# Optimization experiments

Measured on AMD Instinct MI355X. Metric: run time of the kernel, lower is better.

Reference implementation:

```python
import jax, jax.numpy as jnp
import numpy as np

N_NODES = 100000
N_EDGES = 1600000
IN_CH = 128
NF = 128
OUT_CH = 3
N_LAYERS = 7
SLOPE = 0.02


def _glorot(key, shape):
    fan_in = shape[-1]
    bound = 1.0 / np.sqrt(fan_in)
    return jax.random.uniform(key, shape, jnp.float32, -bound, bound)


def setup_inputs() -> dict:
    key = jax.random.key(0)
    ks = jax.random.split(key, 10)
    x = jax.random.normal(ks[0], (N_NODES, IN_CH), jnp.float32)
    edge_index = jax.random.randint(ks[1], (2, N_EDGES), 0, N_NODES, jnp.int64 if jax.config.jax_enable_x64 else jnp.int32)
    # 7 hidden SAGEConv layers (in=128 == nf=128, so stackable)
    Wl = _glorot(ks[2], (N_LAYERS, NF, NF))   # neighbor-branch weight (lin_l)
    bl = jnp.zeros((N_LAYERS, NF), jnp.float32)
    Wr = _glorot(ks[3], (N_LAYERS, NF, NF))   # root weight (lin_r, no bias)
    # output SAGEConv: nf -> out_channels
    Wl_out = _glorot(ks[4], (OUT_CH, NF))
    bl_out = jnp.zeros((OUT_CH,), jnp.float32)
    Wr_out = _glorot(ks[5], (OUT_CH, NF))
    return {"x": x, "edge_index": edge_index, "Wl": Wl, "bl": bl, "Wr": Wr,
            "Wl_out": Wl_out, "bl_out": bl_out, "Wr_out": Wr_out}


def _leaky(v):
    return jnp.where(v >= 0, v, SLOPE * v)


def _sage_conv(h, src, dst, Wl, bl, Wr, n_nodes):
    # max-aggregate neighbor features: gather x_j = h[src], scatter-max into dst
    agg = jax.ops.segment_max(h[src], dst, num_segments=n_nodes)  # [N, C]
    agg = jnp.where(jnp.isneginf(agg), 0.0, agg)  # isolated nodes -> 0 (PyG convention)
    return agg @ Wl.T + bl + h @ Wr.T


def reference(x, edge_index, Wl, bl, Wr, Wl_out, bl_out, Wr_out):
    n = x.shape[0]
    src, dst = edge_index[0], edge_index[1]
    h = x
    # PyG BasicGNN: activation between layers, none after the last conv
    for i in range(N_LAYERS):
        h = _sage_conv(h, src, dst, Wl[i], bl[i], Wr[i], n)
        if i < N_LAYERS - 1:
            h = _leaky(h)
    # wrapper: leaky_relu, dropout (eval -> identity), final SAGEConv, tanh*0.5
    h = _leaky(h)
    h = _sage_conv(h, src, dst, Wl_out, bl_out, Wr_out, n)
    return jnp.tanh(h) * 0.5
```

## Files before the change

kernel.cpp:

```cpp
#include <hip/hip_runtime.h>
#include <hip/hip_bf16.h>
#include <math.h>

#define NN 100000
#define NE 1600000
#define NFE 128
#define SCAN_NB 98

using f32x4 = __attribute__((ext_vector_type(4))) float;
using s16x8 = __attribute__((ext_vector_type(8))) short;
using s16x4 = __attribute__((ext_vector_type(4))) short;

__device__ __forceinline__ short bf16_rne(float x) {
  unsigned u = __float_as_uint(x);
  unsigned r = u + 0x7FFFu + ((u >> 16) & 1u);
  return (short)(r >> 16);
}
__device__ __forceinline__ float bf16_f(short s) {
  return __uint_as_float(((unsigned)(unsigned short)s) << 16);
}
__device__ __forceinline__ float leaky(float v) {
  return v >= 0.0f ? v : 0.02f * v;
}
__device__ __forceinline__ float4 fmax4(float4 a, float4 b) {
  return make_float4(fmaxf(a.x, b.x), fmaxf(a.y, b.y), fmaxf(a.z, b.z), fmaxf(a.w, b.w));
}


__global__ __launch_bounds__(256) void k_zero_i32(int* __restrict__ p, int n) {
  int i = blockIdx.x * blockDim.x + threadIdx.x;
  if (i < n) p[i] = 0;
}

__global__ __launch_bounds__(256) void k_hist(const int* __restrict__ dst,
                                              int* __restrict__ counts) {
  int e = blockIdx.x * blockDim.x + threadIdx.x;
  if (e < NE) atomicAdd(&counts[dst[e]], 1);
}

__global__ __launch_bounds__(256) void k_scan_sum(const int* __restrict__ counts,
                                                  int* __restrict__ bsum) {
  const int t = threadIdx.x;
  const int base = blockIdx.x * 1024 + t * 4;
  int4 c = make_int4(0, 0, 0, 0);
  if (base + 3 < NN) c = *(const int4*)(counts + base);
  else {
    if (base + 0 < NN) c.x = counts[base + 0];
    if (base + 1 < NN) c.y = counts[base + 1];
    if (base + 2 < NN) c.z = counts[base + 2];
  }
  int s = c.x + c.y + c.z + c.w;
#pragma unroll
  for (int off = 32; off; off >>= 1) s += __shfl_down(s, off, 64);
  __shared__ int ws[4];
  if ((t & 63) == 0) ws[t >> 6] = s;
  __syncthreads();
  if (t == 0) bsum[blockIdx.x] = ws[0] + ws[1] + ws[2] + ws[3];
}

__global__ __launch_bounds__(128) void k_scan_top(const int* __restrict__ bsum,
                                                  int* __restrict__ boff) {
  __shared__ int v[128];
  const int t = threadIdx.x;
  int mine = (t < SCAN_NB) ? bsum[t] : 0;
  v[t] = mine;
  __syncthreads();
  for (int off = 1; off < 128; off <<= 1) {
    int u = (t >= off) ? v[t - off] : 0;
    __syncthreads();
    v[t] += u;
    __syncthreads();
  }
  if (t < SCAN_NB) boff[t] = v[t] - mine;
}

__global__ __launch_bounds__(256) void k_scan_blk(const int* __restrict__ counts,
                                                  const int* __restrict__ boff,
                                                  int* __restrict__ row_ptr,
                                                  int* __restrict__ cursor) {
  __shared__ int part[256];
  const int t = threadIdx.x;
  const int base = blockIdx.x * 1024 + t * 4;
  int4 c = make_int4(0, 0, 0, 0);
  if (base + 3 < NN) c = *(const int4*)(counts + base);
  else {
    if (base + 0 < NN) c.x = counts[base + 0];
    if (base + 1 < NN) c.y = counts[base + 1];
    if (base + 2 < NN) c.z = counts[base + 2];
  }
  const int s = c.x + c.y + c.z + c.w;
  part[t] = s;
  __syncthreads();
  for (int off = 1; off < 256; off <<= 1) {
    int u = (t >= off) ? part[t - off] : 0;
    __syncthreads();
    part[t] += u;
    __syncthreads();
  }
  int excl = boff[blockIdx.x] + part[t] - s;
  int4 r;
  r.x = excl;
  r.y = r.x + c.x;
  r.z = r.y + c.y;
  r.w = r.z + c.z;
  const int4 z = make_int4(0, 0, 0, 0);
  if (base + 3 < NN) {
    *(int4*)(row_ptr + base) = r;
    *(int4*)(cursor + base) = z;
  } else {
    if (base + 0 < NN) { row_ptr[base + 0] = r.x; cursor[base + 0] = 0; }
    if (base + 1 < NN) { row_ptr[base + 1] = r.y; cursor[base + 1] = 0; }
    if (base + 2 < NN) { row_ptr[base + 2] = r.z; cursor[base + 2] = 0; }
  }
  if (blockIdx.x == 0 && t == 0) row_ptr[NN] = NE;
}

__global__ __launch_bounds__(256) void k_fill(const int* __restrict__ src,
                                              const int* __restrict__ dst,
                                              const int* __restrict__ row_ptr,
                                              int* __restrict__ cursor,
                                              int* __restrict__ nbr) {
  int e = blockIdx.x * blockDim.x + threadIdx.x;
  if (e >= NE) return;
  int d = dst[e];
  int p = atomicAdd(&cursor[d], 1);
  nbr[row_ptr[d] + p] = src[e];
}


__global__ __launch_bounds__(256) void k_prep_w(const float* __restrict__ Wl,
                                                const float* __restrict__ Wr,
                                                short* __restrict__ wb) {
  int idx = blockIdx.x * 256 + threadIdx.x;
  if (idx >= 7 * 2 * 16384) return;
  int li = idx / 32768;
  int rem = idx % 32768;
  int seg = rem / 16384;
  int ok = rem % 16384;
  float v = seg ? Wr[li * 16384 + ok] : Wl[li * 16384 + ok];
  short hi = bf16_rne(v);
  short lo = bf16_rne(v - bf16_f(hi));
  short* base = wb + (size_t)li * 65536 + seg * 32768;
  base[ok] = hi;
  base[16384 + ok] = lo;
}


__global__ __launch_bounds__(256) void k_layer_fused(const float* __restrict__ hin,
                                                     const int* __restrict__ row_ptr,
                                                     const int* __restrict__ nbr,
                                                     const short* __restrict__ wbl,
                                                     const float* __restrict__ bl,
                                                     float* __restrict__ hout) {
  __shared__ __align__(16) char smem[4 * 8192];
  const int t = threadIdx.x;
  const int base = blockIdx.x * 32;

  {
    char* dhi = smem + 2 * 8192;
    char* dlo = smem + 3 * 8192;
#pragma unroll
    for (int i = 0; i < 2; ++i) {
      int c = t + 256 * i;
      int row = c >> 4;
      int kc = (c & 15) * 8;
      const float4* g = (const float4*)(hin + (size_t)(base + row) * NFE + kc);
      float4 v0 = g[0], v1 = g[1];
      float f[8] = {v0.x, v0.y, v0.z, v0.w, v1.x, v1.y, v1.z, v1.w};
      s16x8 hv, lv;
#pragma unroll
      for (int j = 0; j < 8; ++j) {
        short h = bf16_rne(f[j]);
        hv[j] = h;
        lv[j] = bf16_rne(f[j] - bf16_f(h));
      }
      int off = row * 256 + kc * 2;
      off ^= (row & 7) << 4;
      *(s16x8*)(dhi + off) = hv;
      *(s16x8*)(dlo + off) = lv;
    }
  }

  {
    char* ahi = smem;
    char* alo = smem + 8192;
    const int grp = t >> 5;
    const int lg = t & 31;
    const int c4 = lg << 2;
    const float NI = __int_as_float(0xFF800000);
#pragma unroll
    for (int ni = 0; ni < 4; ++ni) {
      const int r = grp * 4 + ni;
      const int n = base + r;
      const int start = row_ptr[n], end = row_ptr[n + 1];
      float4 acc = make_float4(NI, NI, NI, NI);
      int j = start;
      for (; j + 4 <= end; j += 4) {
        int s0 = nbr[j], s1 = nbr[j + 1], s2 = nbr[j + 2], s3 = nbr[j + 3];
        float4 v0 = *(const float4*)(hin + (size_t)s0 * NFE + c4);
        float4 v1 = *(const float4*)(hin + (size_t)s1 * NFE + c4);
        float4 v2 = *(const float4*)(hin + (size_t)s2 * NFE + c4);
        float4 v3 = *(const float4*)(hin + (size_t)s3 * NFE + c4);
        acc = fmax4(acc, fmax4(fmax4(v0, v1), fmax4(v2, v3)));
      }
      for (; j < end; ++j) {
        int s = nbr[j];
        acc = fmax4(acc, *(const float4*)(hin + (size_t)s * NFE + c4));
      }
      if (start == end) acc = make_float4(0.f, 0.f, 0.f, 0.f);
      float f[4] = {acc.x, acc.y, acc.z, acc.w};
      s16x4 hv, lv;
#pragma unroll
      for (int q = 0; q < 4; ++q) {
        short h = bf16_rne(f[q]);
        hv[q] = h;
        lv[q] = bf16_rne(f[q] - bf16_f(h));
      }
      int off = r * 256 + c4 * 2;
      off ^= (r & 7) << 4;
      *(s16x4*)(ahi + off) = hv;
      *(s16x4*)(alo + off) = lv;
    }
  }
  __syncthreads();

  const int w = t >> 6;
  const int l = t & 63;
  const int lr = l & 15;
  const int lk = (l >> 4) * 8;

  f32x4 acc[2][2] = {};

#pragma unroll
  for (int seg = 0; seg < 2; ++seg) {
    const char* ahi = smem + (seg * 2 + 0) * 8192;
    const char* alo = smem + (seg * 2 + 1) * 8192;
    const short* bhb = wbl + seg * 32768;
    const short* blb = wbl + seg * 32768 + 16384;
#pragma unroll
    for (int ks = 0; ks < 4; ++ks) {
      const int k0 = ks * 32;
      int offa0 = (lr) * 256 + (k0 + lk) * 2;      offa0 ^= ((lr) & 7) << 4;
      int offa1 = (16 + lr) * 256 + (k0 + lk) * 2; offa1 ^= ((16 + lr) & 7) << 4;
      s16x8 ah0 = *(const s16x8*)(ahi + offa0);
      s16x8 ah1 = *(const s16x8*)(ahi + offa1);
      s16x8 al0 = *(const s16x8*)(alo + offa0);
      s16x8 al1 = *(const s16x8*)(alo + offa1);
#pragma unroll
      for (int ct = 0; ct < 2; ++ct) {
        const int col = w * 32 + ct * 16 + lr;
        const s16x8 bh = *(const s16x8*)(bhb + col * 128 + k0 + lk);
        const s16x8 bl_ = *(const s16x8*)(blb + col * 128 + k0 + lk);
        acc[0][ct] = __builtin_amdgcn_mfma_f32_16x16x32_bf16(ah0, bh, acc[0][ct], 0, 0, 0);
        acc[1][ct] = __builtin_amdgcn_mfma_f32_16x16x32_bf16(ah1, bh, acc[1][ct], 0, 0, 0);
        acc[0][ct] = __builtin_amdgcn_mfma_f32_16x16x32_bf16(ah0, bl_, acc[0][ct], 0, 0, 0);
        acc[1][ct] = __builtin_amdgcn_mfma_f32_16x16x32_bf16(ah1, bl_, acc[1][ct], 0, 0, 0);
        acc[0][ct] = __builtin_amdgcn_mfma_f32_16x16x32_bf16(al0, bh, acc[0][ct], 0, 0, 0);
        acc[1][ct] = __builtin_amdgcn_mfma_f32_16x16x32_bf16(al1, bh, acc[1][ct], 0, 0, 0);
      }
    }
  }

  const float bias0 = bl[w * 32 + lr];
  const float bias1 = bl[w * 32 + 16 + lr];
#pragma unroll
  for (int rt = 0; rt < 2; ++rt) {
#pragma unroll
    for (int r = 0; r < 4; ++r) {
      int node = base + 16 * rt + (l >> 4) * 4 + r;
      float* o = hout + (size_t)node * NFE + w * 32;
      o[lr]      = leaky(acc[rt][0][r] + bias0);
      o[16 + lr] = leaky(acc[rt][1][r] + bias1);
    }
  }
}


__global__ __launch_bounds__(256) void k_final_fused(const float* __restrict__ h,
                                                     const int* __restrict__ row_ptr,
                                                     const int* __restrict__ nbr,
                                                     const float* __restrict__ Wlo,
                                                     const float* __restrict__ blo,
                                                     const float* __restrict__ Wro,
                                                     float* __restrict__ out) {
  const int wave = threadIdx.x >> 6;
  const int lane = threadIdx.x & 63;
  const int n = blockIdx.x * 4 + wave;
  if (n >= NN) return;
  const int c2 = lane * 2;
  const int start = row_ptr[n], end = row_ptr[n + 1];
  const float NI = __int_as_float(0xFF800000);
  float ax = NI, ay = NI;
  int j = start;
  for (; j + 4 <= end; j += 4) {
    int s0 = nbr[j], s1 = nbr[j + 1], s2 = nbr[j + 2], s3 = nbr[j + 3];
    float2 v0 = *(const float2*)(h + (size_t)s0 * NFE + c2);
    float2 v1 = *(const float2*)(h + (size_t)s1 * NFE + c2);
    float2 v2 = *(const float2*)(h + (size_t)s2 * NFE + c2);
    float2 v3 = *(const float2*)(h + (size_t)s3 * NFE + c2);
    ax = fmaxf(ax, fmaxf(fmaxf(v0.x, v1.x), fmaxf(v2.x, v3.x)));
    ay = fmaxf(ay, fmaxf(fmaxf(v0.y, v1.y), fmaxf(v2.y, v3.y)));
  }
  for (; j < end; ++j) {
    float2 v = *(const float2*)(h + (size_t)nbr[j] * NFE + c2);
    ax = fmaxf(ax, v.x);
    ay = fmaxf(ay, v.y);
  }
  if (start == end) { ax = 0.f; ay = 0.f; }
  const float2 hv = *(const float2*)(h + (size_t)n * NFE + c2);
  float p[3];
#pragma unroll
  for (int o = 0; o < 3; ++o) {
    const float2 wl = *(const float2*)(Wlo + o * NFE + c2);
    const float2 wr = *(const float2*)(Wro + o * NFE + c2);
    p[o] = ax * wl.x + ay * wl.y + hv.x * wr.x + hv.y * wr.y;
#pragma unroll
    for (int off = 32; off; off >>= 1) p[o] += __shfl_down(p[o], off, 64);
  }
  if (lane == 0) {
#pragma unroll
    for (int o = 0; o < 3; ++o)
      out[(size_t)n * 3 + o] = tanhf(p[o] + blo[o]) * 0.5f;
  }
}


extern "C" void kernel_launch(void* const* d_in, const int* in_sizes, int n_in,
                              void* d_out, int out_size, void* d_ws, size_t ws_size,
                              hipStream_t stream) {
  const float* x   = (const float*)d_in[0];
  const int*   ei  = (const int*)d_in[1];
  const float* Wl  = (const float*)d_in[2];
  const float* bl  = (const float*)d_in[3];
  const float* Wr  = (const float*)d_in[4];
  const float* Wlo = (const float*)d_in[5];
  const float* blo = (const float*)d_in[6];
  const float* Wro = (const float*)d_in[7];
  float* out = (float*)d_out;

  const int* src = ei;
  const int* dst = ei + NE;

  char* ws = (char*)d_ws;
  size_t off = 0;
  auto alloc = [&](size_t bytes) { void* p = ws + off; off = (off + bytes + 255) & ~(size_t)255; return p; };
  int* counts  = (int*)alloc(sizeof(int) * NN);
  int* cursor  = (int*)alloc(sizeof(int) * NN);
  int* row_ptr = (int*)alloc(sizeof(int) * (NN + 1));
  int* nbr     = (int*)alloc(sizeof(int) * NE);
  int* bsum    = (int*)alloc(sizeof(int) * 128);
  int* boff    = (int*)alloc(sizeof(int) * 128);
  short* wb    = (short*)alloc(sizeof(short) * 7 * 65536);
  const size_t hbytes = (size_t)NN * NFE * sizeof(float);
  float* hA  = (float*)alloc(hbytes);
  float* hB  = (float*)alloc(hbytes);

  const int EB = (NE + 255) / 256;

  k_prep_w<<<(7 * 32768 + 255) / 256, 256, 0, stream>>>(Wl, Wr, wb);
  k_zero_i32<<<(NN + 255) / 256, 256, 0, stream>>>(counts, NN);
  k_hist<<<EB, 256, 0, stream>>>(dst, counts);
  k_scan_sum<<<SCAN_NB, 256, 0, stream>>>(counts, bsum);
  k_scan_top<<<1, 128, 0, stream>>>(bsum, boff);
  k_scan_blk<<<SCAN_NB, 256, 0, stream>>>(counts, boff, row_ptr, cursor);
  k_fill<<<EB, 256, 0, stream>>>(src, dst, row_ptr, cursor, nbr);

  const float* hin = x;
  float* bufs[2] = {hA, hB};
  for (int i = 0; i < 7; ++i) {
    float* hout = bufs[i & 1];
    k_layer_fused<<<NN / 32, 256, 0, stream>>>(hin, row_ptr, nbr,
                                               wb + (size_t)i * 65536,
                                               bl + (size_t)i * NFE, hout);
    hin = hout;
  }

  k_final_fused<<<(NN + 3) / 4, 256, 0, stream>>>(hin, row_ptr, nbr, Wlo, blo, Wro, out);
}
```

Baseline: 1.448 ms.

## Halve LDS in fused SAGE layer, load root features directly from global

The root (self) feature tile is no longer staged in shared memory. Each wave reads its MFMA A-fragments straight from global memory and splits them into bf16 hi/lo in registers, which halves LDS use to 16KB, and launch bounds now request 8 blocks per CU. The neighbor max-gather is remapped so that 8 threads cover one node with 16 channels each, replacing 32 threads per node with 4 channels each, and the gather loop is unrolled by 2. The aim is higher occupancy and wider per-thread loads, at the cost of redundant global reads of the root tile across the 4 waves and more registers per thread.

```diff
diff --git a/kernel.cpp b/kernel.cpp
--- a/kernel.cpp
+++ b/kernel.cpp
@@ -9,7 +9,6 @@
 
 using f32x4 = __attribute__((ext_vector_type(4))) float;
 using s16x8 = __attribute__((ext_vector_type(8))) short;
-using s16x4 = __attribute__((ext_vector_type(4))) short;
 
 __device__ __forceinline__ short bf16_rne(float x) {
   unsigned u = __float_as_uint(x);
@@ -146,81 +145,67 @@
 }
 
 
-__global__ __launch_bounds__(256) void k_layer_fused(const float* __restrict__ hin,
-                                                     const int* __restrict__ row_ptr,
-                                                     const int* __restrict__ nbr,
-                                                     const short* __restrict__ wbl,
-                                                     const float* __restrict__ bl,
-                                                     float* __restrict__ hout) {
-  __shared__ __align__(16) char smem[4 * 8192];
+__global__ __launch_bounds__(256, 8) void k_layer_fused(const float* __restrict__ hin,
+                                                        const int* __restrict__ row_ptr,
+                                                        const int* __restrict__ nbr,
+                                                        const short* __restrict__ wbl,
+                                                        const float* __restrict__ bl,
+                                                        float* __restrict__ hout) {
+  __shared__ __align__(16) char smem[2 * 8192];
   const int t = threadIdx.x;
   const int base = blockIdx.x * 32;
-
-  {
-    char* dhi = smem + 2 * 8192;
-    char* dlo = smem + 3 * 8192;
-#pragma unroll
-    for (int i = 0; i < 2; ++i) {
-      int c = t + 256 * i;
-      int row = c >> 4;
-      int kc = (c & 15) * 8;
-      const float4* g = (const float4*)(hin + (size_t)(base + row) * NFE + kc);
-      float4 v0 = g[0], v1 = g[1];
-      float f[8] = {v0.x, v0.y, v0.z, v0.w, v1.x, v1.y, v1.z, v1.w};
-      s16x8 hv, lv;
-#pragma unroll
-      for (int j = 0; j < 8; ++j) {
-        short h = bf16_rne(f[j]);
-        hv[j] = h;
-        lv[j] = bf16_rne(f[j] - bf16_f(h));
-      }
-      int off = row * 256 + kc * 2;
-      off ^= (row & 7) << 4;
-      *(s16x8*)(dhi + off) = hv;
-      *(s16x8*)(dlo + off) = lv;
-    }
-  }
 
   {
     char* ahi = smem;
     char* alo = smem + 8192;
-    const int grp = t >> 5;
-    const int lg = t & 31;
-    const int c4 = lg << 2;
+    const int r = t >> 3;
+    const int lg = t & 7;
+    const int c0 = lg * 16;
+    const int n = base + r;
+    const int start = row_ptr[n], end = row_ptr[n + 1];
     const float NI = __int_as_float(0xFF800000);
-#pragma unroll
-    for (int ni = 0; ni < 4; ++ni) {
-      const int r = grp * 4 + ni;
-      const int n = base + r;
-      const int start = row_ptr[n], end = row_ptr[n + 1];
-      float4 acc = make_float4(NI, NI, NI, NI);
-      int j = start;
-      for (; j + 4 <= end; j += 4) {
-        int s0 = nbr[j], s1 = nbr[j + 1], s2 = nbr[j + 2], s3 = nbr[j + 3];
-        float4 v0 = *(const float4*)(hin + (size_t)s0 * NFE + c4);
-        float4 v1 = *(const float4*)(hin + (size_t)s1 * NFE + c4);
-        float4 v2 = *(const float4*)(hin + (size_t)s2 * NFE + c4);
-        float4 v3 = *(const float4*)(hin + (size_t)s3 * NFE + c4);
-        acc = fmax4(acc, fmax4(fmax4(v0, v1), fmax4(v2, v3)));
-      }
-      for (; j < end; ++j) {
-        int s = nbr[j];
-        acc = fmax4(acc, *(const float4*)(hin + (size_t)s * NFE + c4));
-      }
-      if (start == end) acc = make_float4(0.f, 0.f, 0.f, 0.f);
-      float f[4] = {acc.x, acc.y, acc.z, acc.w};
-      s16x4 hv, lv;
-#pragma unroll
-      for (int q = 0; q < 4; ++q) {
-        short h = bf16_rne(f[q]);
-        hv[q] = h;
-        lv[q] = bf16_rne(f[q] - bf16_f(h));
-      }
-      int off = r * 256 + c4 * 2;
-      off ^= (r & 7) << 4;
-      *(s16x4*)(ahi + off) = hv;
-      *(s16x4*)(alo + off) = lv;
-    }
+    float4 a0 = make_float4(NI, NI, NI, NI), a1 = a0, a2 = a0, a3 = a0;
+    int j = start;
+    for (; j + 2 <= end; j += 2) {
+      int s0 = nbr[j], s1 = nbr[j + 1];
+      const float4* p0 = (const float4*)(hin + (size_t)s0 * NFE + c0);
+      const float4* p1 = (const float4*)(hin + (size_t)s1 * NFE + c0);
+      float4 u0 = p0[0], u1 = p0[1], u2 = p0[2], u3 = p0[3];
+      float4 w0 = p1[0], w1 = p1[1], w2 = p1[2], w3 = p1[3];
+      a0 = fmax4(a0, fmax4(u0, w0));
+      a1 = fmax4(a1, fmax4(u1, w1));
+      a2 = fmax4(a2, fmax4(u2, w2));
+      a3 = fmax4(a3, fmax4(u3, w3));
+    }
+    if (j < end) {
+      const float4* p0 = (const float4*)(hin + (size_t)nbr[j] * NFE + c0);
+      a0 = fmax4(a0, p0[0]);
+      a1 = fmax4(a1, p0[1]);
+      a2 = fmax4(a2, p0[2]);
+      a3 = fmax4(a3, p0[3]);
+    }
+    if (start == end) {
+      a0 = make_float4(0.f, 0.f, 0.f, 0.f);
+      a1 = a0; a2 = a0; a3 = a0;
+    }
+    float f[16] = {a0.x, a0.y, a0.z, a0.w, a1.x, a1.y, a1.z, a1.w,
+                   a2.x, a2.y, a2.z, a2.w, a3.x, a3.y, a3.z, a3.w};
+    s16x8 hv0, hv1, lv0, lv1;
+#pragma unroll
+    for (int q = 0; q < 8; ++q) {
+      short h0 = bf16_rne(f[q]);
+      hv0[q] = h0;
+      lv0[q] = bf16_rne(f[q] - bf16_f(h0));
+      short h1 = bf16_rne(f[q + 8]);
+      hv1[q] = h1;
+      lv1[q] = bf16_rne(f[q + 8] - bf16_f(h1));
+    }
+    const int ob = r * 256 + c0 * 2;
+    const int sw = (r & 7) << 4;
+    *(s16x8*)(ahi + (ob ^ sw))        = hv0;
+    *(s16x8*)(ahi + ((ob + 16) ^ sw)) = hv1;
+    *(s16x8*)(alo + (ob ^ sw))        = lv0;
+    *(s16x8*)(alo + ((ob + 16) ^ sw)) = lv1;
   }
   __syncthreads();
 
@@ -233,19 +218,40 @@
 
 #pragma unroll
   for (int seg = 0; seg < 2; ++seg) {
-    const char* ahi = smem + (seg * 2 + 0) * 8192;
-    const char* alo = smem + (seg * 2 + 1) * 8192;
     const short* bhb = wbl + seg * 32768;
     const short* blb = wbl + seg * 32768 + 16384;
 #pragma unroll
     for (int ks = 0; ks < 4; ++ks) {
       const int k0 = ks * 32;
-      int offa0 = (lr) * 256 + (k0 + lk) * 2;      offa0 ^= ((lr) & 7) << 4;
-      int offa1 = (16 + lr) * 256 + (k0 + lk) * 2; offa1 ^= ((16 + lr) & 7) << 4;
-      s16x8 ah0 = *(const s16x8*)(ahi + offa0);
-      s16x8 ah1 = *(const s16x8*)(ahi + offa1);
-      s16x8 al0 = *(const s16x8*)(alo + offa0);
-      s16x8 al1 = *(const s16x8*)(alo + offa1);
+      s16x8 ah0, ah1, al0, al1;
+      if (seg == 0) {
+        const char* ahi = smem;
+        const char* alo = smem + 8192;
+        int offa0 = (lr) * 256 + (k0 + lk) * 2;      offa0 ^= ((lr) & 7) << 4;
+        int offa1 = (16 + lr) * 256 + (k0 + lk) * 2; offa1 ^= ((16 + lr) & 7) << 4;
+        ah0 = *(const s16x8*)(smem + offa0);
+        ah1 = *(const s16x8*)(smem + offa1);
+        al0 = *(const s16x8*)(alo + offa0);
+        al1 = *(const s16x8*)(alo + offa1);
+        (void)ahi;
+      } else {
+#pragma unroll
+        for (int rt = 0; rt < 2; ++rt) {
+          const float* gp = hin + (size_t)(base + rt * 16 + lr) * NFE + k0 + lk;
+          float4 g0 = *(const float4*)(gp);
+          float4 g1 = *(const float4*)(gp + 4);
+          float f[8] = {g0.x, g0.y, g0.z, g0.w, g1.x, g1.y, g1.z, g1.w};
+          s16x8 hv, lv;
+#pragma unroll
+          for (int q = 0; q < 8; ++q) {
+            short h = bf16_rne(f[q]);
+            hv[q] = h;
+            lv[q] = bf16_rne(f[q] - bf16_f(h));
+          }
+          if (rt == 0) { ah0 = hv; al0 = lv; }
+          else         { ah1 = hv; al1 = lv; }
+        }
+      }
 #pragma unroll
       for (int ct = 0; ct < 2; ++ct) {
         const int col = w * 32 + ct * 16 + lr;
```

Result: slower. 1.585 ms (+9.4%).

## Warp-specialize layer kernel into persistent gather/MFMA producer-consumer pipeline

Applied to the files above, without the earlier changes.

Replaces the one-tile-per-block layer kernel with a persistent 512-thread kernel on a fixed grid. Four waves gather neighbors, max-aggregate and split to bf16 hi/lo into a double-buffered LDS tile. The other four waves run the MFMA GEMM and epilogue on the previous tile. The goal is to overlap the latency-bound gather with matrix-core work, at the cost of per-tile block barriers, a fixed 512-block grid that may load-balance unevenly, and half the threads idle during each phase.

```diff
diff --git a/kernel.cpp b/kernel.cpp
--- a/kernel.cpp
+++ b/kernel.cpp
@@ -6,6 +6,8 @@
 #define NE 1600000
 #define NFE 128
 #define SCAN_NB 98
+#define NT_TOTAL 3125
+#define PIPE_GRID 512
 
 using f32x4 = __attribute__((ext_vector_type(4))) float;
 using s16x8 = __attribute__((ext_vector_type(8))) short;
@@ -146,131 +148,148 @@
 }
 
 
-__global__ __launch_bounds__(256) void k_layer_fused(const float* __restrict__ hin,
-                                                     const int* __restrict__ row_ptr,
-                                                     const int* __restrict__ nbr,
-                                                     const short* __restrict__ wbl,
-                                                     const float* __restrict__ bl,
-                                                     float* __restrict__ hout) {
-  __shared__ __align__(16) char smem[4 * 8192];
+__global__ __launch_bounds__(512, 4) void k_layer_pipe(const float* __restrict__ hin,
+                                                       const int* __restrict__ row_ptr,
+                                                       const int* __restrict__ nbr,
+                                                       const short* __restrict__ wbl,
+                                                       const float* __restrict__ bl,
+                                                       float* __restrict__ hout) {
+  __shared__ __align__(16) char smem[2 * 32768];
   const int t = threadIdx.x;
-  const int base = blockIdx.x * 32;
-
-  {
-    char* dhi = smem + 2 * 8192;
-    char* dlo = smem + 3 * 8192;
-#pragma unroll
-    for (int i = 0; i < 2; ++i) {
-      int c = t + 256 * i;
-      int row = c >> 4;
-      int kc = (c & 15) * 8;
-      const float4* g = (const float4*)(hin + (size_t)(base + row) * NFE + kc);
-      float4 v0 = g[0], v1 = g[1];
-      float f[8] = {v0.x, v0.y, v0.z, v0.w, v1.x, v1.y, v1.z, v1.w};
-      s16x8 hv, lv;
-#pragma unroll
-      for (int j = 0; j < 8; ++j) {
-        short h = bf16_rne(f[j]);
-        hv[j] = h;
-        lv[j] = bf16_rne(f[j] - bf16_f(h));
-      }
-      int off = row * 256 + kc * 2;
-      off ^= (row & 7) << 4;
-      *(s16x8*)(dhi + off) = hv;
-      *(s16x8*)(dlo + off) = lv;
-    }
-  }
-
-  {
-    char* ahi = smem;
-    char* alo = smem + 8192;
-    const int grp = t >> 5;
-    const int lg = t & 31;
+  const int wave = t >> 6;
+  const int bid = blockIdx.x;
+  const int nt = (NT_TOTAL - bid + PIPE_GRID - 1) / PIPE_GRID;
+
+  if (wave < 4) {
+    const int pt = t;
+    const int srow = pt >> 3;
+    const int sc0 = (pt & 7) * 16;
+    const int grp = pt >> 5;
+    const int lg = pt & 31;
     const int c4 = lg << 2;
     const float NI = __int_as_float(0xFF800000);
-#pragma unroll
-    for (int ni = 0; ni < 4; ++ni) {
-      const int r = grp * 4 + ni;
-      const int n = base + r;
-      const int start = row_ptr[n], end = row_ptr[n + 1];
-      float4 acc = make_float4(NI, NI, NI, NI);
-      int j = start;
-      for (; j + 4 <= end; j += 4) {
-        int s0 = nbr[j], s1 = nbr[j + 1], s2 = nbr[j + 2], s3 = nbr[j + 3];
-        float4 v0 = *(const float4*)(hin + (size_t)s0 * NFE + c4);
-        float4 v1 = *(const float4*)(hin + (size_t)s1 * NFE + c4);
-        float4 v2 = *(const float4*)(hin + (size_t)s2 * NFE + c4);
-        float4 v3 = *(const float4*)(hin + (size_t)s3 * NFE + c4);
-        acc = fmax4(acc, fmax4(fmax4(v0, v1), fmax4(v2, v3)));
+
+    for (int s = 0; s < nt; ++s) {
+      const int base = (bid + s * PIPE_GRID) * 32;
+      char* buf = smem + (s & 1) * 32768;
+      char* aggHi = buf;
+      char* aggLo = buf + 8192;
+      char* hinHi = buf + 16384;
+      char* hinLo = buf + 24576;
+
+      {
+        const float4* g = (const float4*)(hin + (size_t)(base + srow) * NFE + sc0);
+        float4 v0 = g[0], v1 = g[1], v2 = g[2], v3 = g[3];
+        float f[16] = {v0.x, v0.y, v0.z, v0.w, v1.x, v1.y, v1.z, v1.w,
+                       v2.x, v2.y, v2.z, v2.w, v3.x, v3.y, v3.z, v3.w};
+        s16x8 hv0, hv1, lv0, lv1;
+#pragma unroll
+        for (int q = 0; q < 8; ++q) {
+          short h0 = bf16_rne(f[q]);
+          hv0[q] = h0;
+          lv0[q] = bf16_rne(f[q] - bf16_f(h0));
+          short h1 = bf16_rne(f[q + 8]);
+          hv1[q] = h1;
+          lv1[q] = bf16_rne(f[q + 8] - bf16_f(h1));
+        }
+        const int ob = srow * 256 + sc0 * 2;
+        const int sw = (srow & 7) << 4;
+        *(s16x8*)(hinHi + (ob ^ sw))        = hv0;
+        *(s16x8*)(hinHi + ((ob + 16) ^ sw)) = hv1;
+        *(s16x8*)(hinLo + (ob ^ sw))        = lv0;
+        *(s16x8*)(hinLo + ((ob + 16) ^ sw)) = lv1;
       }
-      for (; j < end; ++j) {
-        int s = nbr[j];
-        acc = fmax4(acc, *(const float4*)(hin + (size_t)s * NFE + c4));
+
+#pragma unroll
+      for (int ni = 0; ni < 4; ++ni) {
+        const int r = grp * 4 + ni;
+        const int n = base + r;
+        const int start = row_ptr[n], end = row_ptr[n + 1];
+        float4 acc = make_float4(NI, NI, NI, NI);
+        int j = start;
+        for (; j + 4 <= end; j += 4) {
+          int s0 = nbr[j], s1 = nbr[j + 1], s2 = nbr[j + 2], s3 = nbr[j + 3];
+          float4 v0 = *(const float4*)(hin + (size_t)s0 * NFE + c4);
+          float4 v1 = *(const float4*)(hin + (size_t)s1 * NFE + c4);
+          float4 v2 = *(const float4*)(hin + (size_t)s2 * NFE + c4);
+          float4 v3 = *(const float4*)(hin + (size_t)s3 * NFE + c4);
+          acc = fmax4(acc, fmax4(fmax4(v0, v1), fmax4(v2, v3)));
+        }
+        for (; j < end; ++j) {
+          acc = fmax4(acc, *(const float4*)(hin + (size_t)nbr[j] * NFE + c4));
+        }
+        if (start == end) acc = make_float4(0.f, 0.f, 0.f, 0.f);
+        float f[4] = {acc.x, acc.y, acc.z, acc.w};
+        s16x4 hv, lv;
+#pragma unroll
+        for (int q = 0; q < 4; ++q) {
+          short h = bf16_rne(f[q]);
+          hv[q] = h;
+          lv[q] = bf16_rne(f[q] - bf16_f(h));
+        }
+        int off = r * 256 + c4 * 2;
+        off ^= (r & 7) << 4;
+        *(s16x4*)(aggHi + off) = hv;
+        *(s16x4*)(aggLo + off) = lv;
       }
-      if (start == end) acc = make_float4(0.f, 0.f, 0.f, 0.f);
-      float f[4] = {acc.x, acc.y, acc.z, acc.w};
-      s16x4 hv, lv;
-#pragma unroll
-      for (int q = 0; q < 4; ++q) {
-        short h = bf16_rne(f[q]);
-        hv[q] = h;
-        lv[q] = bf16_rne(f[q] - bf16_f(h));
+      __syncthreads();
+    }
+    __syncthreads();
+  } else {
+    const int w = wave - 4;
+    const int l = t & 63;
+    const int lr = l & 15;
+    const int lk = (l >> 4) * 8;
+
+    __syncthreads();
+    for (int s = 1; s <= nt; ++s) {
+      const int base = (bid + (s - 1) * PIPE_GRID) * 32;
+      const char* buf = smem + ((s - 1) & 1) * 32768;
+
+      f32x4 acc[2][2] = {};
+#pragma unroll
+      for (int seg = 0; seg < 2; ++seg) {
+        const char* ahiB = buf + seg * 16384;
+        const char* aloB = ahiB + 8192;
+        const short* bhb = wbl + seg * 32768;
+        const short* blb = bhb + 16384;
+#pragma unroll
+        for (int ks = 0; ks < 4; ++ks) {
+          const int k0 = ks * 32;
+          int offa0 = (lr) * 256 + (k0 + lk) * 2;      offa0 ^= ((lr) & 7) << 4;
+          int offa1 = (16 + lr) * 256 + (k0 + lk) * 2; offa1 ^= ((16 + lr) & 7) << 4;
+          s16x8 ah0 = *(const s16x8*)(ahiB + offa0);
+          s16x8 ah1 = *(const s16x8*)(ahiB + offa1);
+          s16x8 al0 = *(const s16x8*)(aloB + offa0);
+          s16x8 al1 = *(const s16x8*)(aloB + offa1);
+#pragma unroll
+          for (int ct = 0; ct < 2; ++ct) {
+            const int col = w * 32 + ct * 16 + lr;
+            const s16x8 bh = *(const s16x8*)(bhb + col * 128 + k0 + lk);
+            const s16x8 bl_ = *(const s16x8*)(blb + col * 128 + k0 + lk);
+            acc[0][ct] = __builtin_amdgcn_mfma_f32_16x16x32_bf16(ah0, bh, acc[0][ct], 0, 0, 0);
+            acc[1][ct] = __builtin_amdgcn_mfma_f32_16x16x32_bf16(ah1, bh, acc[1][ct], 0, 0, 0);
+            acc[0][ct] = __builtin_amdgcn_mfma_f32_16x16x32_bf16(ah0, bl_, acc[0][ct], 0, 0, 0);
+            acc[1][ct] = __builtin_amdgcn_mfma_f32_16x16x32_bf16(ah1, bl_, acc[1][ct], 0, 0, 0);
+            acc[0][ct] = __builtin_amdgcn_mfma_f32_16x16x32_bf16(al0, bh, acc[0][ct], 0, 0, 0);
+            acc[1][ct] = __builtin_amdgcn_mfma_f32_16x16x32_bf16(al1, bh, acc[1][ct], 0, 0, 0);
+          }
+        }
       }
-      int off = r * 256 + c4 * 2;
-      off ^= (r & 7) << 4;
-      *(s16x4*)(ahi + off) = hv;
-      *(s16x4*)(alo + off) = lv;
-    }
-  }
-  __syncthreads();
-
-  const int w = t >> 6;
-  const int l = t & 63;
-  const int lr = l & 15;
-  const int lk = (l >> 4) * 8;
-
-  f32x4 acc[2][2] = {};
-
-#pragma unroll
-  for (int seg = 0; seg < 2; ++seg) {
-    const char* ahi = smem + (seg * 2 + 0) * 8192;
-    const char* alo = smem + (seg * 2 + 1) * 8192;
-    const short* bhb = wbl + seg * 32768;
-    const short* blb = wbl + seg * 32768 + 16384;
-#pragma unroll
-    for (int ks = 0; ks < 4; ++ks) {
-      const int k0 = ks * 32;
-      int offa0 = (lr) * 256 + (k0 + lk) * 2;      offa0 ^= ((lr) & 7) << 4;
-      int offa1 = (16 + lr) * 256 + (k0 + lk) * 2; offa1 ^= ((16 + lr) & 7) << 4;
-      s16x8 ah0 = *(const s16x8*)(ahi + offa0);
-      s16x8 ah1 = *(const s16x8*)(ahi + offa1);
-      s16x8 al0 = *(const s16x8*)(alo + offa0);
-      s16x8 al1 = *(const s16x8*)(alo + offa1);
-#pragma unroll
-      for (int ct = 0; ct < 2; ++ct) {
-        const int col = w * 32 + ct * 16 + lr;
-        const s16x8 bh = *(const s16x8*)(bhb + col * 128 + k0 + lk);
-        const s16x8 bl_ = *(const s16x8*)(blb + col * 128 + k0 + lk);
-        acc[0][ct] = __builtin_amdgcn_mfma_f32_16x16x32_bf16(ah0, bh, acc[0][ct], 0, 0, 0);
-        acc[1][ct] = __builtin_amdgcn_mfma_f32_16x16x32_bf16(ah1, bh, acc[1][ct], 0, 0, 0);
-        acc[0][ct] = __builtin_amdgcn_mfma_f32_16x16x32_bf16(ah0, bl_, acc[0][ct], 0, 0, 0);
-        acc[1][ct] = __builtin_amdgcn_mfma_f32_16x16x32_bf16(ah1, bl_, acc[1][ct], 0, 0, 0);
-        acc[0][ct] = __builtin_amdgcn_mfma_f32_16x16x32_bf16(al0, bh, acc[0][ct], 0, 0, 0);
-        acc[1][ct] = __builtin_amdgcn_mfma_f32_16x16x32_bf16(al1, bh, acc[1][ct], 0, 0, 0);
+
+      const float bias0 = bl[w * 32 + lr];
+      const float bias1 = bl[w * 32 + 16 + lr];
+#pragma unroll
+      for (int rt = 0; rt < 2; ++rt) {
+#pragma unroll
+        for (int r = 0; r < 4; ++r) {
+          int node = base + 16 * rt + (l >> 4) * 4 + r;
+          float* o = hout + (size_t)node * NFE + w * 32;
+          o[lr]      = leaky(acc[rt][0][r] + bias0);
+          o[16 + lr] = leaky(acc[rt][1][r] + bias1);
+        }
       }
-    }
-  }
-
-  const float bias0 = bl[w * 32 + lr];
-  const float bias1 = bl[w * 32 + 16 + lr];
-#pragma unroll
-  for (int rt = 0; rt < 2; ++rt) {
-#pragma unroll
-    for (int r = 0; r < 4; ++r) {
-      int node = base + 16 * rt + (l >> 4) * 4 + r;
-      float* o = hout + (size_t)node * NFE + w * 32;
-      o[lr]      = leaky(acc[rt][0][r] + bias0);
-      o[16 + lr] = leaky(acc[rt][1][r] + bias1);
+      __syncthreads();
     }
   }
 }
@@ -369,9 +388,9 @@
   float* bufs[2] = {hA, hB};
   for (int i = 0; i < 7; ++i) {
     float* hout = bufs[i & 1];
-    k_layer_fused<<<NN / 32, 256, 0, stream>>>(hin, row_ptr, nbr,
-                                               wb + (size_t)i * 65536,
-                                               bl + (size_t)i * NFE, hout);
+    k_layer_pipe<<<PIPE_GRID, 512, 0, stream>>>(hin, row_ptr, nbr,
+                                                wb + (size_t)i * 65536,
+                                                bl + (size_t)i * NFE, hout);
     hin = hout;
   }
 
```

Result: slower. 1.515 ms (+4.6%).
